# Kernel tuning notes

Hardware: AMD Instinct MI355X
Metric: run time of the kernel (lower is better)

The kernel has to match this reference:

```python
import jax, jax.numpy as jnp
import numpy as np

N_NODES, N_EDGES, N_PAIRS, FEAT, N_LAYERS = 10000, 160000, 8, 64, 2


def setup_inputs() -> dict:
    key = jax.random.key(0)
    ks = jax.random.split(key, 12)
    s = 1.0 / np.sqrt(FEAT)
    x = jax.random.normal(ks[0], (N_NODES, FEAT), jnp.float32)
    # distinct node ids so unique(pos) has exactly 2*N_PAIRS elements (static B)
    pos = jax.random.permutation(ks[1], N_NODES)[: 2 * N_PAIRS].reshape(N_PAIRS, 2).astype(jnp.int32)
    edge_src = jax.random.randint(ks[2], (N_EDGES,), 0, N_NODES, jnp.int32)
    edge_dst = jax.random.randint(ks[3], (N_EDGES,), 0, N_NODES, jnp.int32)
    edge_weight = jax.random.uniform(ks[4], (N_EDGES,), jnp.float32)
    f0_w = jax.random.normal(ks[5], (N_LAYERS, FEAT, FEAT), jnp.float32) * s
    f0_b = jax.random.normal(ks[6], (N_LAYERS, FEAT), jnp.float32) * 0.01
    f1_w = jax.random.normal(ks[7], (N_LAYERS, FEAT, FEAT), jnp.float32) * s
    f1_b = jax.random.normal(ks[8], (N_LAYERS, FEAT), jnp.float32) * 0.01
    conv_w = jax.random.normal(ks[9], (N_LAYERS, FEAT, FEAT), jnp.float32) * s
    conv_b = jax.random.normal(ks[10], (N_LAYERS, FEAT), jnp.float32) * 0.01
    return {"x": x, "pos": pos, "edge_src": edge_src, "edge_dst": edge_dst,
            "edge_weight": edge_weight, "f0_w": f0_w, "f0_b": f0_b,
            "f1_w": f1_w, "f1_b": f1_b, "conv_w": conv_w, "conv_b": conv_b}


def reference(x, pos, edge_src, edge_dst, edge_weight, f0_w, f0_b, f1_w, f1_b, conv_w, conv_b):
    N = x.shape[0]
    M = pos.shape[0]
    B = 2 * M  # pos entries are distinct -> B unique labeled nodes (static)
    L = f0_w.shape[0]
    # convert_pos: sel_id = unique labeled nodes, ret = flat index into (B*N)
    sel_id, inv = jnp.unique(pos, return_inverse=True, size=B, fill_value=0)
    inv = inv.reshape(pos.shape)
    ret = pos + inv[:, ::-1] * N  # (M,2): pair (u,v) -> x0[batch_of_v, u], x0[batch_of_u, v]
    idx0 = jnp.arange(B)

    h = x  # layer 0: (N,F); later layers: (B,N,H)
    for i in range(L):
        if i == 0:
            base = h @ f0_w[0] + f0_b[0]                         # (N,H)
            x0 = jnp.broadcast_to(base, (B,) + base.shape)       # (B,N,H)
            x1 = h[sel_id] @ f1_w[0] + f1_b[0]                   # (B,H)
        else:
            x0 = h @ f0_w[i] + f0_b[i]                           # (B,N,H)
            x1 = h[idx0, sel_id] @ f1_w[i] + f1_b[i]             # (B,H)
        x0 = x0.at[idx0, sel_id].set(x1)  # scatter labeled-node embeddings
        # sparse adjacency conv: aggregate over edges, then linear
        xT = jnp.swapaxes(x0, 0, 1)                              # (N,B,H)
        msgs = xT[edge_src] * edge_weight[:, None, None]         # (E,B,H)
        agg = jax.ops.segment_sum(msgs, edge_dst, num_segments=N)  # (N,B,H)
        h = jnp.swapaxes(agg, 0, 1) @ conv_w[i] + conv_b[i]      # (B,N,H)
        if i < L - 1:
            h = jax.nn.relu(h)
    flat = h.reshape(B * N, -1)
    return flat[ret]  # (M, 2, H)
```

## Files before the change

kernel.cpp:

```cpp
#include <hip/hip_runtime.h>

#define F 64
#define SECAP 8192
#define TCAP 2048
#define FCAP 8256
#define BLK 256
#define EPIW 4

struct Params {
  const float *x, *ew, *f0w, *f0b, *f1w, *f1b, *cw, *cb;
  const int *pos, *esrc, *edst;
  float *out;
  int B, E;
  int *cnt;
  int *TEn;
  unsigned *bitmap;
  int *sel, *slotb, *slot_of, *SEb, *SEd, *TEsrc2;
  float *SEw, *TEw2, *AGG, *wsum, *zf;
};

__device__ __forceinline__ void mark_assign(const Params& p, int n) {
  unsigned bit = 1u << (n & 31);
  unsigned old = atomicOr(&p.bitmap[n >> 5], bit);
  if (!(old & bit)) {
    int sl = atomicAdd(&p.cnt[2], 1);
    if (sl < FCAP) {
      p.slot_of[n] = sl;
      float4* row = (float4*)(p.AGG + (size_t)sl * F);
#pragma unroll
      for (int k = 0; k < 16; ++k) row[k] = make_float4(0.f, 0.f, 0.f, 0.f);
      p.wsum[sl] = 0.f;
    } else {
      p.slot_of[n] = 0;
    }
  }
}

__global__ __launch_bounds__(BLK) void kp_scan(Params p) {
  __shared__ int posL[16], rankL[16];
  const int tid = threadIdx.x;
  const int B = p.B;
  if (tid < B) {
    int v = p.pos[tid];
    int rank = 0;
    for (int j = 0; j < B; ++j) rank += (p.pos[j] < v);
    posL[tid] = v;
    rankL[tid] = rank;
  }
  __syncthreads();
  if (blockIdx.x == 0 && tid < B) {
    p.sel[rankL[tid]] = posL[tid];
    p.slotb[tid] = rankL[tid ^ 1];
    mark_assign(p, posL[tid]);
  }
  int gtid = blockIdx.x * BLK + tid;
  int nthr = gridDim.x * BLK;
  for (int e = gtid; e < p.E; e += nthr) {
    int s = p.esrc[e], d = p.edst[e];
    float w = p.ew[e];
    int bi = -1, ti = -1;
#pragma unroll
    for (int j = 0; j < 16; ++j) {
      if (j < B) {
        if (s == posL[j]) bi = rankL[j];
        if (d == posL[j]) ti = j;
      }
    }
    if (bi >= 0) {
      int idx = atomicAdd(&p.cnt[0], 1);
      if (idx < SECAP) { p.SEb[idx] = bi; p.SEd[idx] = d; p.SEw[idx] = w; }
    }
    if (ti >= 0) {
      int idx = atomicAdd(&p.TEn[ti], 1);
      if (idx < TCAP) { p.TEsrc2[ti * TCAP + idx] = s; p.TEw2[ti * TCAP + idx] = w; }
      mark_assign(p, s);
    }
  }
}

__global__ __launch_bounds__(BLK) void kp_agg(Params p) {
  int gtid = blockIdx.x * BLK + threadIdx.x;
  int nthr = gridDim.x * BLK;
  for (int e = gtid; e < p.E; e += nthr) {
    int d = p.edst[e];
    if (!((p.bitmap[d >> 5] >> (d & 31)) & 1u)) continue;
    int sl = p.slot_of[d];
    if ((unsigned)sl >= (unsigned)FCAP) continue;
    int s = p.esrc[e];
    float w = p.ew[e];
    const float4* xs = (const float4*)(p.x + (size_t)s * F);
    float* dst = p.AGG + (size_t)sl * F;
#pragma unroll
    for (int k = 0; k < 16; ++k) {
      float4 v = xs[k];
      atomicAdd(dst + 4 * k + 0, w * v.x);
      atomicAdd(dst + 4 * k + 1, w * v.y);
      atomicAdd(dst + 4 * k + 2, w * v.z);
      atomicAdd(dst + 4 * k + 3, w * v.w);
    }
    atomicAdd(&p.wsum[sl], w);
  }
}

#define MVB(res, init, vecp, mat)                         \
  {                                                       \
    float a0_ = 0.f, a1_ = 0.f, a2_ = 0.f, a3_ = 0.f;     \
    _Pragma("unroll")                                     \
    for (int q_ = 0; q_ < 16; ++q_) {                     \
      float4 vv_ = ((const float4*)(vecp))[q_];           \
      a0_ += vv_.x * (mat)[(4 * q_ + 0) * 64 + h];        \
      a1_ += vv_.y * (mat)[(4 * q_ + 1) * 64 + h];        \
      a2_ += vv_.z * (mat)[(4 * q_ + 2) * 64 + h];        \
      a3_ += vv_.w * (mat)[(4 * q_ + 3) * 64 + h];        \
    }                                                     \
    res = (init) + ((a0_ + a1_) + (a2_ + a3_));           \
  }

__global__ __launch_bounds__(BLK) void kp_zf(Params p) {
  __shared__ __align__(16) float a[4][64], tt[4][64];
  const int Fn = min(p.cnt[2], FCAP);
  const int ty = threadIdx.x >> 6, h = threadIdx.x & 63;
  for (int sl = blockIdx.x * 4 + ty; sl < Fn; sl += gridDim.x * 4) {
    a[ty][h] = p.AGG[(size_t)sl * F + h];
    float t1;
    MVB(t1, p.wsum[sl] * p.f0b[h], a[ty], p.f0w);
    tt[ty][h] = t1;
    float z;
    MVB(z, p.cb[h], tt[ty], p.cw);
    p.zf[(size_t)sl * F + h] = z;
  }
}

__global__ __launch_bounds__(BLK) void kp_epi(Params p) {
  __shared__ float cL[FCAP];
  __shared__ __align__(16) float v0[EPIW][64], v1[EPIW][64];
  __shared__ __align__(16) float Sp[EPIW][64];
  __shared__ float wnsL[EPIW], wselL[EPIW];
  __shared__ int slL[TCAP];
  __shared__ float twL[TCAP];
  const int t = blockIdx.x;
  const int tid = threadIdx.x;
  const int h = tid & 63, wv = tid >> 6;
  const int b = p.slotb[t];
  const int seln = p.sel[b];
  const int Fn = min(p.cnt[2], FCAP);
  for (int i = tid; i < Fn; i += BLK) cL[i] = 0.f;
  __syncthreads();
  int sen = min(p.cnt[0], SECAP);
  for (int i = tid; i < sen; i += BLK) {
    if (p.SEb[i] == b) {
      int d = p.SEd[i];
      if ((p.bitmap[d >> 5] >> (d & 31)) & 1u) {
        int sl = p.slot_of[d];
        if ((unsigned)sl < (unsigned)FCAP) atomicAdd(&cL[sl], p.SEw[i]);
      }
    }
  }
  int ten = min(p.TEn[t], TCAP);
  for (int i = tid; i < ten; i += BLK) {
    int s = p.TEsrc2[t * TCAP + i];
    int sl;
    if (s == seln) sl = -1;
    else { sl = p.slot_of[s]; if ((unsigned)sl >= (unsigned)FCAP) sl = 0; }
    slL[i] = sl;
    twL[i] = p.TEw2[t * TCAP + i];
  }
  __syncthreads();
  v0[wv][h] = p.x[(size_t)seln * F + h];
  float d0h;
  {
    float a0_ = 0.f, a1_ = 0.f, a2_ = 0.f, a3_ = 0.f;
#pragma unroll
    for (int q = 0; q < 16; ++q) {
      float4 vv = ((const float4*)(v0[wv]))[q];
      a0_ += vv.x * (p.f1w[(4 * q + 0) * 64 + h] - p.f0w[(4 * q + 0) * 64 + h]);
      a1_ += vv.y * (p.f1w[(4 * q + 1) * 64 + h] - p.f0w[(4 * q + 1) * 64 + h]);
      a2_ += vv.z * (p.f1w[(4 * q + 2) * 64 + h] - p.f0w[(4 * q + 2) * 64 + h]);
      a3_ += vv.w * (p.f1w[(4 * q + 3) * 64 + h] - p.f0w[(4 * q + 3) * 64 + h]);
    }
    d0h = (p.f1b[h] - p.f0b[h]) + ((a0_ + a1_) + (a2_ + a3_));
  }
  v0[wv][h] = d0h;
  float g0h;
  MVB(g0h, 0.f, v0[wv], p.cw);
  int sslot = p.slot_of[seln];
  if ((unsigned)sslot >= (unsigned)FCAP) sslot = 0;
  float h1self = fmaxf(p.zf[(size_t)sslot * F + h] + cL[sslot] * g0h, 0.f);
  v0[wv][h] = h1self;
  float x11h;
  MVB(x11h, p.f1b[64 + h], v0[wv], (p.f1w + 4096));
  float S = 0.f, wns = 0.f, wsel = 0.f;
  for (int i = wv; i < ten; i += EPIW) {
    int sl = slL[i];
    float w = twL[i];
    if (sl < 0) { wsel += w; continue; }
    float h1 = fmaxf(p.zf[(size_t)sl * F + h] + cL[sl] * g0h, 0.f);
    S += w * h1;
    wns += w;
  }
  Sp[wv][h] = S;
  if (h == 0) { wnsL[wv] = wns; wselL[wv] = wsel; }
  __syncthreads();
  if (wv == 0) {
    float Sh = Sp[0][h] + Sp[1][h] + Sp[2][h] + Sp[3][h];
    float wnsT = wnsL[0] + wnsL[1] + wnsL[2] + wnsL[3];
    float wselT = wselL[0] + wselL[1] + wselL[2] + wselL[3];
    v0[0][h] = Sh;
    float a2h;
    MVB(a2h, wnsT * p.f0b[64 + h] + wselT * x11h, v0[0], (p.f0w + 4096));
    v1[0][h] = a2h;
    float o;
    MVB(o, p.cb[64 + h], v1[0], (p.cw + 4096));
    p.out[t * F + h] = o;
  }
}

extern "C" void kernel_launch(void* const* d_in, const int* in_sizes, int n_in,
                              void* d_out, int out_size, void* d_ws, size_t ws_size,
                              hipStream_t stream) {
  Params hp;
  hp.x = (const float*)d_in[0];
  hp.pos = (const int*)d_in[1];
  hp.esrc = (const int*)d_in[2];
  hp.edst = (const int*)d_in[3];
  hp.ew = (const float*)d_in[4];
  hp.f0w = (const float*)d_in[5];
  hp.f0b = (const float*)d_in[6];
  hp.f1w = (const float*)d_in[7];
  hp.f1b = (const float*)d_in[8];
  hp.cw = (const float*)d_in[9];
  hp.cb = (const float*)d_in[10];
  hp.out = (float*)d_out;
  const int N = in_sizes[0] / F;
  hp.B = in_sizes[1];
  hp.E = in_sizes[2];

  char* w = (char*)d_ws;
  size_t off = 0;
  auto take = [&](size_t nb) { size_t r = off; off += (nb + 255) & ~(size_t)255; return r; };
  size_t o_cnt = take(256);
  size_t o_ten = take(256);
  size_t o_bitmap = take(((size_t)N + 31) / 32 * 4);
  size_t zero_end = off;
  size_t o_sel = take(256);
  size_t o_slotb = take(256);
  size_t o_slotof = take((size_t)N * 4);
  size_t o_seb = take(SECAP * 4);
  size_t o_sed = take(SECAP * 4);
  size_t o_sew = take(SECAP * 4);
  size_t o_tesrc = take((size_t)hp.B * TCAP * 4);
  size_t o_tew = take((size_t)hp.B * TCAP * 4);
  size_t o_agg = take((size_t)FCAP * F * 4);
  size_t o_wsum = take((size_t)FCAP * 4);
  size_t o_zf = take((size_t)FCAP * F * 4);
  (void)ws_size;

  hp.cnt = (int*)(w + o_cnt);
  hp.TEn = (int*)(w + o_ten);
  hp.bitmap = (unsigned*)(w + o_bitmap);
  hp.sel = (int*)(w + o_sel);
  hp.slotb = (int*)(w + o_slotb);
  hp.slot_of = (int*)(w + o_slotof);
  hp.SEb = (int*)(w + o_seb);
  hp.SEd = (int*)(w + o_sed);
  hp.SEw = (float*)(w + o_sew);
  hp.TEsrc2 = (int*)(w + o_tesrc);
  hp.TEw2 = (float*)(w + o_tew);
  hp.AGG = (float*)(w + o_agg);
  hp.wsum = (float*)(w + o_wsum);
  hp.zf = (float*)(w + o_zf);

  hipMemsetAsync(d_ws, 0, zero_end, stream);
  int nbE = (hp.E + BLK - 1) / BLK;
  if (nbE > 2048) nbE = 2048;
  kp_scan<<<nbE, BLK, 0, stream>>>(hp);
  kp_agg<<<nbE, BLK, 0, stream>>>(hp);
  kp_zf<<<256, BLK, 0, stream>>>(hp);
  kp_epi<<<hp.B, BLK, 0, stream>>>(hp);
  (void)n_in; (void)out_size;
}
```

Measured before the change: 55.88 us.

## Prefold chained weight products and vectorize edge scans with int4 loads

Extra blocks in the scan kernel precompute the products of consecutive weight matrices (f0w·cw, (f1w−f0w)·cw, f1w1·cw1, f0w1·cw1) and the matching bias vectors. The zf and epilogue kernels then do one matrix-vector product where they used to do two. The scan and aggregation kernels now read edge arrays as int4/float4, four edges per thread, so they launch a quarter as many blocks. The zf grid is halved. Folding the matrices changes the floating-point summation order slightly and adds a small GEMM prologue to the scan kernel.

```diff
diff --git a/kernel.cpp b/kernel.cpp
--- a/kernel.cpp
+++ b/kernel.cpp
@@ -17,6 +17,8 @@
   unsigned *bitmap;
   int *sel, *slotb, *slot_of, *SEb, *SEd, *TEsrc2;
   float *SEw, *TEw2, *AGG, *wsum, *zf;
+  float *P0, *G, *V, *Wp;
+  float *b0c, *gb, *vb, *wpb;
 };
 
 __device__ __forceinline__ void mark_assign(const Params& p, int n) {
@@ -33,72 +35,6 @@
     } else {
       p.slot_of[n] = 0;
     }
-  }
-}
-
-__global__ __launch_bounds__(BLK) void kp_scan(Params p) {
-  __shared__ int posL[16], rankL[16];
-  const int tid = threadIdx.x;
-  const int B = p.B;
-  if (tid < B) {
-    int v = p.pos[tid];
-    int rank = 0;
-    for (int j = 0; j < B; ++j) rank += (p.pos[j] < v);
-    posL[tid] = v;
-    rankL[tid] = rank;
-  }
-  __syncthreads();
-  if (blockIdx.x == 0 && tid < B) {
-    p.sel[rankL[tid]] = posL[tid];
-    p.slotb[tid] = rankL[tid ^ 1];
-    mark_assign(p, posL[tid]);
-  }
-  int gtid = blockIdx.x * BLK + tid;
-  int nthr = gridDim.x * BLK;
-  for (int e = gtid; e < p.E; e += nthr) {
-    int s = p.esrc[e], d = p.edst[e];
-    float w = p.ew[e];
-    int bi = -1, ti = -1;
-#pragma unroll
-    for (int j = 0; j < 16; ++j) {
-      if (j < B) {
-        if (s == posL[j]) bi = rankL[j];
-        if (d == posL[j]) ti = j;
-      }
-    }
-    if (bi >= 0) {
-      int idx = atomicAdd(&p.cnt[0], 1);
-      if (idx < SECAP) { p.SEb[idx] = bi; p.SEd[idx] = d; p.SEw[idx] = w; }
-    }
-    if (ti >= 0) {
-      int idx = atomicAdd(&p.TEn[ti], 1);
-      if (idx < TCAP) { p.TEsrc2[ti * TCAP + idx] = s; p.TEw2[ti * TCAP + idx] = w; }
-      mark_assign(p, s);
-    }
-  }
-}
-
-__global__ __launch_bounds__(BLK) void kp_agg(Params p) {
-  int gtid = blockIdx.x * BLK + threadIdx.x;
-  int nthr = gridDim.x * BLK;
-  for (int e = gtid; e < p.E; e += nthr) {
-    int d = p.edst[e];
-    if (!((p.bitmap[d >> 5] >> (d & 31)) & 1u)) continue;
-    int sl = p.slot_of[d];
-    if ((unsigned)sl >= (unsigned)FCAP) continue;
-    int s = p.esrc[e];
-    float w = p.ew[e];
-    const float4* xs = (const float4*)(p.x + (size_t)s * F);
-    float* dst = p.AGG + (size_t)sl * F;
-#pragma unroll
-    for (int k = 0; k < 16; ++k) {
-      float4 v = xs[k];
-      atomicAdd(dst + 4 * k + 0, w * v.x);
-      atomicAdd(dst + 4 * k + 1, w * v.y);
-      atomicAdd(dst + 4 * k + 2, w * v.z);
-      atomicAdd(dst + 4 * k + 3, w * v.w);
-    }
-    atomicAdd(&p.wsum[sl], w);
   }
 }
 
@@ -116,24 +52,145 @@
     res = (init) + ((a0_ + a1_) + (a2_ + a3_));           \
   }
 
+__global__ __launch_bounds__(BLK) void kp_scan(Params p, int nbE) {
+  const int tid = threadIdx.x;
+  if ((int)blockIdx.x >= nbE) {
+    __shared__ __align__(16) float Al[64][64];
+    const int ty = tid >> 6, h = tid & 63;
+    int wb = blockIdx.x - nbE;
+    if (wb < 4) {
+      const float *A, *A2 = nullptr, *Bm;
+      float* Om;
+      if (wb == 0)      { A = p.f0w;        Bm = p.cw;        Om = p.P0; }
+      else if (wb == 1) { A = p.f1w;        A2 = p.f0w; Bm = p.cw; Om = p.G; }
+      else if (wb == 2) { A = p.f1w + 4096; Bm = p.cw + 4096; Om = p.V; }
+      else              { A = p.f0w + 4096; Bm = p.cw + 4096; Om = p.Wp; }
+      for (int i = tid; i < 4096; i += BLK)
+        Al[i >> 6][i & 63] = A2 ? (A[i] - A2[i]) : A[i];
+      __syncthreads();
+      float acc[16];
+#pragma unroll
+      for (int fi = 0; fi < 16; ++fi) acc[fi] = 0.f;
+      for (int k = 0; k < 64; ++k) {
+        float bkh = Bm[k * 64 + h];
+#pragma unroll
+        for (int fi = 0; fi < 16; ++fi)
+          acc[fi] += Al[ty * 16 + fi][k] * bkh;
+      }
+#pragma unroll
+      for (int fi = 0; fi < 16; ++fi)
+        Om[(ty * 16 + fi) * 64 + h] = acc[fi];
+    } else {
+      const float *vsrc, *v2 = nullptr, *Bm;
+      float* Ov;
+      if (ty == 0)      { vsrc = p.f0b;      Bm = p.cw;        Ov = p.b0c; }
+      else if (ty == 1) { vsrc = p.f1b;      v2 = p.f0b; Bm = p.cw; Ov = p.gb; }
+      else if (ty == 2) { vsrc = p.f1b + 64; Bm = p.cw + 4096; Ov = p.vb; }
+      else              { vsrc = p.f0b + 64; Bm = p.cw + 4096; Ov = p.wpb; }
+      Al[ty][h] = v2 ? (vsrc[h] - v2[h]) : vsrc[h];
+      float acc;
+      MVB(acc, 0.f, Al[ty], Bm);
+      Ov[h] = acc;
+    }
+    return;
+  }
+  __shared__ int posL[16], rankL[16];
+  const int B = p.B;
+  if (tid < B) {
+    int v = p.pos[tid];
+    int rank = 0;
+    for (int j = 0; j < B; ++j) rank += (p.pos[j] < v);
+    posL[tid] = v;
+    rankL[tid] = rank;
+  }
+  __syncthreads();
+  if (blockIdx.x == 0 && tid < B) {
+    p.sel[rankL[tid]] = posL[tid];
+    p.slotb[tid] = rankL[tid ^ 1];
+    mark_assign(p, posL[tid]);
+  }
+  auto proc = [&](int s, int d, float w) {
+    int bi = -1, ti = -1;
+#pragma unroll
+    for (int j = 0; j < 16; ++j) {
+      if (j < B) {
+        if (s == posL[j]) bi = rankL[j];
+        if (d == posL[j]) ti = j;
+      }
+    }
+    if (bi >= 0) {
+      int idx = atomicAdd(&p.cnt[0], 1);
+      if (idx < SECAP) { p.SEb[idx] = bi; p.SEd[idx] = d; p.SEw[idx] = w; }
+    }
+    if (ti >= 0) {
+      int idx = atomicAdd(&p.TEn[ti], 1);
+      if (idx < TCAP) { p.TEsrc2[ti * TCAP + idx] = s; p.TEw2[ti * TCAP + idx] = w; }
+      mark_assign(p, s);
+    }
+  };
+  int gtid = blockIdx.x * BLK + tid;
+  int nthr = nbE * BLK;
+  int nv = p.E >> 2;
+  for (int i = gtid; i < nv; i += nthr) {
+    int4 s4 = ((const int4*)p.esrc)[i];
+    int4 d4 = ((const int4*)p.edst)[i];
+    float4 w4 = ((const float4*)p.ew)[i];
+    proc(s4.x, d4.x, w4.x);
+    proc(s4.y, d4.y, w4.y);
+    proc(s4.z, d4.z, w4.z);
+    proc(s4.w, d4.w, w4.w);
+  }
+  for (int e = (nv << 2) + gtid; e < p.E; e += nthr)
+    proc(p.esrc[e], p.edst[e], p.ew[e]);
+}
+
+__global__ __launch_bounds__(BLK) void kp_agg(Params p) {
+  int gtid = blockIdx.x * BLK + threadIdx.x;
+  int nthr = gridDim.x * BLK;
+  auto proc = [&](int e, int d) {
+    if (!((p.bitmap[d >> 5] >> (d & 31)) & 1u)) return;
+    int sl = p.slot_of[d];
+    if ((unsigned)sl >= (unsigned)FCAP) return;
+    int s = p.esrc[e];
+    float w = p.ew[e];
+    const float4* xs = (const float4*)(p.x + (size_t)s * F);
+    float* dst = p.AGG + (size_t)sl * F;
+#pragma unroll
+    for (int k = 0; k < 16; ++k) {
+      float4 v = xs[k];
+      atomicAdd(dst + 4 * k + 0, w * v.x);
+      atomicAdd(dst + 4 * k + 1, w * v.y);
+      atomicAdd(dst + 4 * k + 2, w * v.z);
+      atomicAdd(dst + 4 * k + 3, w * v.w);
+    }
+    atomicAdd(&p.wsum[sl], w);
+  };
+  int nv = p.E >> 2;
+  for (int i = gtid; i < nv; i += nthr) {
+    int4 d4 = ((const int4*)p.edst)[i];
+    proc(4 * i + 0, d4.x);
+    proc(4 * i + 1, d4.y);
+    proc(4 * i + 2, d4.z);
+    proc(4 * i + 3, d4.w);
+  }
+  for (int e = (nv << 2) + gtid; e < p.E; e += nthr) proc(e, p.edst[e]);
+}
+
 __global__ __launch_bounds__(BLK) void kp_zf(Params p) {
-  __shared__ __align__(16) float a[4][64], tt[4][64];
+  __shared__ __align__(16) float a[4][64];
   const int Fn = min(p.cnt[2], FCAP);
   const int ty = threadIdx.x >> 6, h = threadIdx.x & 63;
   for (int sl = blockIdx.x * 4 + ty; sl < Fn; sl += gridDim.x * 4) {
     a[ty][h] = p.AGG[(size_t)sl * F + h];
-    float t1;
-    MVB(t1, p.wsum[sl] * p.f0b[h], a[ty], p.f0w);
-    tt[ty][h] = t1;
     float z;
-    MVB(z, p.cb[h], tt[ty], p.cw);
+    MVB(z, p.wsum[sl] * p.b0c[h] + p.cb[h], a[ty], p.P0);
     p.zf[(size_t)sl * F + h] = z;
   }
 }
 
 __global__ __launch_bounds__(BLK) void kp_epi(Params p) {
   __shared__ float cL[FCAP];
-  __shared__ __align__(16) float v0[EPIW][64], v1[EPIW][64];
+  __shared__ __align__(16) float v0[EPIW][64];
   __shared__ __align__(16) float Sp[EPIW][64];
   __shared__ float wnsL[EPIW], wselL[EPIW];
   __shared__ int slL[TCAP];
@@ -167,28 +224,14 @@
   }
   __syncthreads();
   v0[wv][h] = p.x[(size_t)seln * F + h];
-  float d0h;
-  {
-    float a0_ = 0.f, a1_ = 0.f, a2_ = 0.f, a3_ = 0.f;
-#pragma unroll
-    for (int q = 0; q < 16; ++q) {
-      float4 vv = ((const float4*)(v0[wv]))[q];
-      a0_ += vv.x * (p.f1w[(4 * q + 0) * 64 + h] - p.f0w[(4 * q + 0) * 64 + h]);
-      a1_ += vv.y * (p.f1w[(4 * q + 1) * 64 + h] - p.f0w[(4 * q + 1) * 64 + h]);
-      a2_ += vv.z * (p.f1w[(4 * q + 2) * 64 + h] - p.f0w[(4 * q + 2) * 64 + h]);
-      a3_ += vv.w * (p.f1w[(4 * q + 3) * 64 + h] - p.f0w[(4 * q + 3) * 64 + h]);
-    }
-    d0h = (p.f1b[h] - p.f0b[h]) + ((a0_ + a1_) + (a2_ + a3_));
-  }
-  v0[wv][h] = d0h;
   float g0h;
-  MVB(g0h, 0.f, v0[wv], p.cw);
+  MVB(g0h, p.gb[h], v0[wv], p.G);
   int sslot = p.slot_of[seln];
   if ((unsigned)sslot >= (unsigned)FCAP) sslot = 0;
   float h1self = fmaxf(p.zf[(size_t)sslot * F + h] + cL[sslot] * g0h, 0.f);
   v0[wv][h] = h1self;
-  float x11h;
-  MVB(x11h, p.f1b[64 + h], v0[wv], (p.f1w + 4096));
+  float x11Th;
+  MVB(x11Th, p.vb[h], v0[wv], p.V);
   float S = 0.f, wns = 0.f, wsel = 0.f;
   for (int i = wv; i < ten; i += EPIW) {
     int sl = slL[i];
@@ -206,11 +249,8 @@
     float wnsT = wnsL[0] + wnsL[1] + wnsL[2] + wnsL[3];
     float wselT = wselL[0] + wselL[1] + wselL[2] + wselL[3];
     v0[0][h] = Sh;
-    float a2h;
-    MVB(a2h, wnsT * p.f0b[64 + h] + wselT * x11h, v0[0], (p.f0w + 4096));
-    v1[0][h] = a2h;
     float o;
-    MVB(o, p.cb[64 + h], v1[0], (p.cw + 4096));
+    MVB(o, wnsT * p.wpb[h] + wselT * x11Th + p.cb[64 + h], v0[0], p.Wp);
     p.out[t * F + h] = o;
   }
 }
@@ -253,6 +293,14 @@
   size_t o_agg = take((size_t)FCAP * F * 4);
   size_t o_wsum = take((size_t)FCAP * 4);
   size_t o_zf = take((size_t)FCAP * F * 4);
+  size_t o_P0 = take(4096 * 4);
+  size_t o_G = take(4096 * 4);
+  size_t o_V = take(4096 * 4);
+  size_t o_Wp = take(4096 * 4);
+  size_t o_b0c = take(256);
+  size_t o_gb = take(256);
+  size_t o_vb = take(256);
+  size_t o_wpb = take(256);
   (void)ws_size;
 
   hp.cnt = (int*)(w + o_cnt);
@@ -269,13 +317,22 @@
   hp.AGG = (float*)(w + o_agg);
   hp.wsum = (float*)(w + o_wsum);
   hp.zf = (float*)(w + o_zf);
+  hp.P0 = (float*)(w + o_P0);
+  hp.G = (float*)(w + o_G);
+  hp.V = (float*)(w + o_V);
+  hp.Wp = (float*)(w + o_Wp);
+  hp.b0c = (float*)(w + o_b0c);
+  hp.gb = (float*)(w + o_gb);
+  hp.vb = (float*)(w + o_vb);
+  hp.wpb = (float*)(w + o_wpb);
 
   hipMemsetAsync(d_ws, 0, zero_end, stream);
-  int nbE = (hp.E + BLK - 1) / BLK;
+  int nbE = ((hp.E >> 2) + BLK - 1) / BLK;
   if (nbE > 2048) nbE = 2048;
-  kp_scan<<<nbE, BLK, 0, stream>>>(hp);
+  if (nbE < 1) nbE = 1;
+  kp_scan<<<nbE + 5, BLK, 0, stream>>>(hp, nbE);
   kp_agg<<<nbE, BLK, 0, stream>>>(hp);
-  kp_zf<<<256, BLK, 0, stream>>>(hp);
+  kp_zf<<<128, BLK, 0, stream>>>(hp);
   kp_epi<<<hp.B, BLK, 0, stream>>>(hp);
   (void)n_in; (void)out_size;
 }
```

New measurement: 68.07 us. 1.22x slower.
